# Kernel tuning notes

Measured on AMD Instinct MI355X. Metric: run time of the kernel, lower is better.

The kernel has to match this reference:

```python
import jax, jax.numpy as jnp
import numpy as np

LOCAL_HEADS = 8
GLOBAL_HEADS = 4
HEAD_DIM = 16  # dim // local_heads


def setup_inputs() -> dict:
    key = jax.random.key(0)
    ks = jax.random.split(key, 6)
    B, N, C = 8, 1024, 128
    gdim = HEAD_DIM * GLOBAL_HEADS  # 64
    return {
        "x": jax.random.normal(ks[0], (B, N, C), dtype=jnp.float32),
        "masks": jax.random.uniform(ks[1], (N, N, 3), dtype=jnp.float32),
        "Wq": jax.random.normal(ks[2], (gdim, C), dtype=jnp.float32) * 0.05,
        "Wk": jax.random.normal(ks[3], (gdim, C), dtype=jnp.float32) * 0.05,
        "Wv": jax.random.normal(ks[4], (C, C), dtype=jnp.float32) * 0.05,
        "mask_proj": jax.random.normal(ks[5], (3, GLOBAL_HEADS * LOCAL_HEADS), dtype=jnp.float32),
    }


def reference(x, masks, Wq, Wk, Wv, mask_proj):
    B, N, C = x.shape
    # projections (torch Linear: y = x @ W.T)
    q = (x @ Wq.T).reshape(B, N, GLOBAL_HEADS, HEAD_DIM)   # [B,N,G,hd]
    k = (x @ Wk.T).reshape(B, N, GLOBAL_HEADS, HEAD_DIM)
    v = (x @ Wv.T).reshape(B, N, LOCAL_HEADS, HEAD_DIM)    # [B,N,L,hd]
    # raw global-head scores: [B,G,N,N]  (no 1/sqrt(d) scaling in original)
    attn = jnp.einsum('bigd,bjgd->bgij', q, k)
    # learned mask mixing: masks [N,N,3] @ mask_proj [3, G*L] -> [N,N,G,L]
    mw = (masks @ mask_proj).reshape(N, N, GLOBAL_HEADS, LOCAL_HEADS)
    # mix global heads into local heads: [B,L,N,N]
    scores = jnp.einsum('bgij,ijgl->blij', attn, mw)
    probs = jax.nn.softmax(scores, axis=-1)               # over keys j
    out = jnp.einsum('blij,bjld->bild', probs, v)         # [B,N,L,hd]
    return out.reshape(B, N, C)
```

## Files before the change

kernel.cpp:

```cpp
#include <hip/hip_runtime.h>

#define BB 8
#define NN 1024
#define CC 128
#define GG 4
#define LL 8
#define GD 64

typedef __attribute__((ext_vector_type(8))) short short8;
typedef __attribute__((ext_vector_type(4))) short short4v;
typedef __attribute__((ext_vector_type(4))) float floatx4;

__device__ __forceinline__ short f2b(float f) {
  union { float f; unsigned u; } c; c.f = f;
  unsigned u = c.u;
  return (short)((u + 0x7FFFu + ((u >> 16) & 1u)) >> 16);
}
__device__ __forceinline__ float b2f(short s) {
  union { unsigned u; float f; } c; c.u = ((unsigned)(unsigned short)s) << 16;
  return c.f;
}
__device__ __forceinline__ void split2(float v, short& hi, short& lo) {
  short h = f2b(v);
  hi = h;
  lo = f2b(v - b2f(h));
}

#if __has_builtin(__builtin_amdgcn_cvt_pk_bf16_f32)
__device__ __forceinline__ unsigned pk2(float a, float b) {
  auto r = __builtin_amdgcn_cvt_pk_bf16_f32(a, b);
  unsigned u; __builtin_memcpy(&u, &r, 4); return u;
}
#else
__device__ __forceinline__ unsigned pk2(float a, float b) {
  return (unsigned)(unsigned short)f2b(a) | ((unsigned)(unsigned short)f2b(b) << 16);
}
#endif

#if __has_builtin(__builtin_amdgcn_exp2f)
#define EXP2(x) __builtin_amdgcn_exp2f(x)
#else
#define EXP2(x) exp2f(x)
#endif

#if __has_builtin(__builtin_amdgcn_global_load_lds)
__device__ __forceinline__ void gll16(const void* g, void* l, int lane) {
  (void)lane;
  __builtin_amdgcn_global_load_lds(
      (const __attribute__((address_space(1))) unsigned int*)g,
      (__attribute__((address_space(3))) unsigned int*)l, 16, 0, 0);
}
#else
__device__ __forceinline__ void gll16(const void* g, void* l, int lane) {
  uint4 t = *(const uint4*)g;
  *(uint4*)((char*)l + lane * 16) = t;
}
#endif

#define BHP 136

__global__ __launch_bounds__(256) void proj_kernel(
    const float* __restrict__ x, const float* __restrict__ Wq,
    const float* __restrict__ Wk, const float* __restrict__ Wv,
    short* __restrict__ qb, short* __restrict__ kb, short* __restrict__ vtb)
{
  __shared__ short bh[64 * BHP];
  __shared__ short bl[64 * BHP];
  const int t = threadIdx.x;
  const int nt = blockIdx.x & 3;
  const int mt = blockIdx.x >> 2;
  const int w = t >> 6;
  const int lane = t & 63;
  const int ln = lane & 15;
  const int hq = lane >> 4;
  const int arow = mt * 64 + w * 16 + ln;

  const float* wbase = (nt == 0) ? Wq : (nt == 1) ? Wk : (Wv + (nt - 2) * 64 * 128);

  {
    int r = t >> 2, c0 = (t & 3) * 32;
    const float* src = wbase + r * 128 + c0;
    #pragma unroll
    for (int z8 = 0; z8 < 4; ++z8) {
      float4 u0 = *(const float4*)(src + z8 * 8);
      float4 u1 = *(const float4*)(src + z8 * 8 + 4);
      float uv[8] = {u0.x,u0.y,u0.z,u0.w,u1.x,u1.y,u1.z,u1.w};
      union { short s[8]; short8 v; } H, L;
      #pragma unroll
      for (int z = 0; z < 8; ++z) split2(uv[z], H.s[z], L.s[z]);
      *(short8*)(bh + r * BHP + c0 + z8 * 8) = H.v;
      *(short8*)(bl + r * BHP + c0 + z8 * 8) = L.v;
    }
  }
  __syncthreads();

  const floatx4 zf = {0.f, 0.f, 0.f, 0.f};
  floatx4 acc[4] = {zf, zf, zf, zf};

  #pragma unroll
  for (int kc = 0; kc < 4; ++kc) {
    const float* xp = x + (long)arow * 128 + kc * 32 + hq * 8;
    float4 a0 = *(const float4*)xp;
    float4 a1 = *(const float4*)(xp + 4);
    union { short s[8]; short8 v; } Ah, Al;
    float av[8] = {a0.x,a0.y,a0.z,a0.w,a1.x,a1.y,a1.z,a1.w};
    #pragma unroll
    for (int z = 0; z < 8; ++z) split2(av[z], Ah.s[z], Al.s[z]);
    #pragma unroll
    for (int ns = 0; ns < 4; ++ns) {
      short8 Bh = *(const short8*)(bh + (ns * 16 + ln) * BHP + kc * 32 + hq * 8);
      short8 Bl = *(const short8*)(bl + (ns * 16 + ln) * BHP + kc * 32 + hq * 8);
      acc[ns] = __builtin_amdgcn_mfma_f32_16x16x32_bf16(Ah.v, Bh, acc[ns], 0,0,0);
      acc[ns] = __builtin_amdgcn_mfma_f32_16x16x32_bf16(Al.v, Bh, acc[ns], 0,0,0);
      acc[ns] = __builtin_amdgcn_mfma_f32_16x16x32_bf16(Ah.v, Bl, acc[ns], 0,0,0);
    }
  }

  if (nt < 2) {
    short* dst = (nt == 0) ? qb : kb;
    #pragma unroll
    for (int ns = 0; ns < 4; ++ns) {
      int col = ns * 16 + ln;
      #pragma unroll
      for (int reg = 0; reg < 4; ++reg) {
        int row = mt * 64 + w * 16 + hq * 4 + reg;
        dst[(long)row * 64 + col] = f2b(acc[ns][reg]);
      }
    }
  } else {
    int b = mt >> 4;
    int tok = (mt * 64 + w * 16 + hq * 4) & 1023;
    #pragma unroll
    for (int ns = 0; ns < 4; ++ns) {
      int cv = (nt - 2) * 64 + ns * 16 + ln;
      union { short s[4]; short4v v; } o;
      #pragma unroll
      for (int reg = 0; reg < 4; ++reg) o.s[reg] = f2b(acc[ns][reg]);
      *(short4v*)(vtb + ((long)b * CC + cv) * NN + tok) = o.v;
    }
  }
}

#define IT 16
#define JT 64
#define SPLIT 2
#define JSPAN 512
#define NTL 8
#define ARP 260
#define MRP 196

__global__ __launch_bounds__(256, 3) void attn_kernel(
    const short* __restrict__ qb, const short* __restrict__ kb,
    const short* __restrict__ vtb, const float* __restrict__ masks,
    const float* __restrict__ mask_proj,
    float* __restrict__ pnum, float* __restrict__ pden)
{
  __shared__ float arec[IT * ARP];
  __shared__ float mrec[IT * MRP];
  __shared__ short kbuf[64 * 64];

  const int t = threadIdx.x;
  const int sp = blockIdx.x & 1;
  const int itile = (blockIdx.x >> 1) & 63;
  const int b = blockIdx.x >> 7;
  const int i0 = itile * IT;

  const int w = t >> 6;
  const int lane = t & 63;
  const int ln = lane & 15;
  const int hq = lane >> 4;
  const int l0 = 2 * w, l1 = 2 * w + 1;

  short8 qf;
  {
    union { short s[8]; short8 v; } qq;
    #pragma unroll
    for (int z = 0; z < 8; ++z) qq.s[z] = 0;
    if (hq < 2)
      qq.v = *(const short8*)(qb + ((long)(b * NN + i0 + ln)) * GD + w * 16 + hq * 8);
    qf = qq.v;
  }
  const float LOG2E = 1.44269504088896340736f;
  float ycA[3][4], ycB[3][4];
  #pragma unroll
  for (int m = 0; m < 3; ++m)
    #pragma unroll
    for (int g = 0; g < 4; ++g) {
      ycA[m][g] = mask_proj[m * 32 + g * 8 + l0] * LOG2E;
      ycB[m][g] = mask_proj[m * 32 + g * 8 + l1] * LOG2E;
    }

  const floatx4 zf = {0.f, 0.f, 0.f, 0.f};
  floatx4 pv0 = zf, pv1 = zf;
  float den0 = 0.f, den1 = 0.f;

  const short* kbase = kb + (long)b * NN * GD;
  const short* v0base = vtb + ((long)b * CC + l0 * 16 + ln) * NN;
  const short* v1base = vtb + ((long)b * CC + l1 * 16 + ln) * NN;

  const int klj = lane >> 3;
  const int ke8 = (lane & 7) ^ klj;

  #pragma unroll
  for (int ii = 0; ii < 2; ++ii) {
    const int I = w * 2 + ii;
    gll16(kbase + (long)(sp * JSPAN + I * 8 + klj) * GD + ke8 * 8,
          kbuf + I * 512, lane);
  }

  for (int jt = 0; jt < NTL; ++jt) {
    const int j0 = sp * JSPAN + jt * JT;
    __syncthreads();

    #pragma unroll
    for (int it2 = 0; it2 < 3; ++it2) {
      int f = t + it2 * 256;
      int ii = f / 48;
      int rem = f - ii * 48;
      *(float4*)(mrec + ii * MRP + rem * 4) =
        *(const float4*)(masks + (long)(i0 + ii) * (NN * 3) + (long)j0 * 3 + rem * 4);
    }
    #pragma unroll
    for (int jsub = 0; jsub < 4; ++jsub) {
      union { short s[8]; short8 v; } kk;
      #pragma unroll
      for (int z = 0; z < 8; ++z) kk.s[z] = 0;
      if (hq < 2) {
        const int jloc = jsub * 16 + ln;
        kk.v = *(const short8*)(kbuf + jloc * 64 + (((w * 2 + hq) ^ (jloc & 7)) << 3));
      }
      floatx4 at = __builtin_amdgcn_mfma_f32_16x16x32_bf16(qf, kk.v, zf, 0, 0, 0);
      float* ab = arec + (jsub * 16 + ln) * 4 + w;
      #pragma unroll
      for (int reg = 0; reg < 4; ++reg)
        ab[(hq * 4 + reg) * ARP] = at[reg];
    }
    __syncthreads();

    {
      const int jn = sp * JSPAN + ((jt + 1) & (NTL - 1)) * JT;
      #pragma unroll
      for (int ii = 0; ii < 2; ++ii) {
        const int I = w * 2 + ii;
        gll16(kbase + (long)(jn + I * 8 + klj) * GD + ke8 * 8,
              kbuf + I * 512, lane);
      }
    }

    #pragma unroll
    for (int mf = 0; mf < 2; ++mf) {
      float mku[24];
      {
        const float* mb = mrec + ln * MRP + mf * 96 + hq * 24;
        #pragma unroll
        for (int q4 = 0; q4 < 6; ++q4)
          *(float4*)(mku + q4 * 4) = *(const float4*)(mb + q4 * 4);
      }
      short8 vf0 = *(const short8*)(v0base + j0 + mf * 32 + hq * 8);
      short8 vf1 = *(const short8*)(v1base + j0 + mf * 32 + hq * 8);
      const float* arA = arec + ln * ARP + (mf * 32 + hq * 8) * 4;
      union { unsigned u[4]; short8 v; } p0, p1;
      #pragma unroll
      for (int zp = 0; zp < 4; ++zp) {
        float eA[2], eB[2];
        #pragma unroll
        for (int zz = 0; zz < 2; ++zz) {
          int z = zp * 2 + zz;
          floatx4 a4 = *(const floatx4*)(arA + z * 4);
          float m0 = mku[z * 3], m1 = mku[z * 3 + 1], m2 = mku[z * 3 + 2];
          float wA0 = m0*ycA[0][0] + m1*ycA[1][0] + m2*ycA[2][0];
          float wA1 = m0*ycA[0][1] + m1*ycA[1][1] + m2*ycA[2][1];
          float wA2 = m0*ycA[0][2] + m1*ycA[1][2] + m2*ycA[2][2];
          float wA3 = m0*ycA[0][3] + m1*ycA[1][3] + m2*ycA[2][3];
          float wB0 = m0*ycB[0][0] + m1*ycB[1][0] + m2*ycB[2][0];
          float wB1 = m0*ycB[0][1] + m1*ycB[1][1] + m2*ycB[2][1];
          float wB2 = m0*ycB[0][2] + m1*ycB[1][2] + m2*ycB[2][2];
          float wB3 = m0*ycB[0][3] + m1*ycB[1][3] + m2*ycB[2][3];
          float sA = a4[0]*wA0 + a4[1]*wA1 + a4[2]*wA2 + a4[3]*wA3;
          float sB = a4[0]*wB0 + a4[1]*wB1 + a4[2]*wB2 + a4[3]*wB3;
          eA[zz] = EXP2(sA);
          eB[zz] = EXP2(sB);
        }
        den0 += eA[0] + eA[1];
        den1 += eB[0] + eB[1];
        p0.u[zp] = pk2(eA[0], eA[1]);
        p1.u[zp] = pk2(eB[0], eB[1]);
      }
      pv0 = __builtin_amdgcn_mfma_f32_16x16x32_bf16(p0.v, vf0, pv0, 0, 0, 0);
      pv1 = __builtin_amdgcn_mfma_f32_16x16x32_bf16(p1.v, vf1, pv1, 0, 0, 0);
    }
  }

  #pragma unroll
  for (int reg = 0; reg < 4; ++reg) {
    long row = ((long)(sp * BB + b)) * NN + i0 + hq * 4 + reg;
    pnum[row * CC + l0 * 16 + ln] = pv0[reg];
    pnum[row * CC + l1 * 16 + ln] = pv1[reg];
  }
  den0 += __shfl_xor(den0, 16, 64);
  den0 += __shfl_xor(den0, 32, 64);
  den1 += __shfl_xor(den1, 16, 64);
  den1 += __shfl_xor(den1, 32, 64);
  if (hq == 0) {
    long drow = ((long)(sp * BB + b)) * NN + i0 + ln;
    pden[drow * LL + l0] = den0;
    pden[drow * LL + l1] = den1;
  }
}

__global__ __launch_bounds__(256) void reduce_kernel(
    const float* __restrict__ pnum, const float* __restrict__ pden,
    float* __restrict__ out)
{
  int e4 = blockIdx.x * 256 + threadIdx.x;
  int bi = e4 >> 5;
  int l = (e4 & 31) >> 2;
  const float4* p4 = (const float4*)pnum;
  float4 n0 = p4[e4];
  float4 n1 = p4[e4 + (BB * NN * CC / 4)];
  float den = pden[(long)bi * LL + l] + pden[((long)BB * NN + bi) * LL + l];
  float inv = 1.0f / den;
  float4 o;
  o.x = (n0.x + n1.x) * inv;
  o.y = (n0.y + n1.y) * inv;
  o.z = (n0.z + n1.z) * inv;
  o.w = (n0.w + n1.w) * inv;
  ((float4*)out)[e4] = o;
}

extern "C" void kernel_launch(void* const* d_in, const int* in_sizes, int n_in,
                              void* d_out, int out_size, void* d_ws, size_t ws_size,
                              hipStream_t stream) {
  const float* x         = (const float*)d_in[0];
  const float* masks     = (const float*)d_in[1];
  const float* Wq        = (const float*)d_in[2];
  const float* Wk        = (const float*)d_in[3];
  const float* Wv        = (const float*)d_in[4];
  const float* mask_proj = (const float*)d_in[5];
  float* out = (float*)d_out;

  char* wsB = (char*)d_ws;
  short* qb   = (short*)(wsB);
  short* kb   = (short*)(wsB + (1l << 20));
  short* vtb  = (short*)(wsB + (2l << 20));
  float* pnum = (float*)(wsB + (4l << 20));
  float* pden = (float*)(wsB + (12l << 20));

  proj_kernel<<<512, 256, 0, stream>>>(x, Wq, Wk, Wv, qb, kb, vtb);
  attn_kernel<<<BB * (NN / IT) * SPLIT, 256, 0, stream>>>(qb, kb, vtb, masks,
                                                          mask_proj, pnum, pden);
  reduce_kernel<<<(BB * NN * CC / 4) / 256, 256, 0, stream>>>(pnum, pden, out);
}
```

Measured before the change: 127.4 us.

## Drop split-K over keys and reduce kernel; use 8 waves per block, one local head each

The attention kernel no longer splits the key range in two with partial numerators and denominators reduced by a separate kernel. Each block now has 512 threads covering the full key range, and each of the 8 waves handles one local head. Waves 4-7 load the mask tile while waves 0-3 compute the QK scores, and the kernel normalizes and writes the output directly. This removes the partial-sum writes, the reduce launch and its traffic, at the cost of half as many blocks and a longer serial loop per block.

```diff
diff --git a/kernel.cpp b/kernel.cpp
--- a/kernel.cpp
+++ b/kernel.cpp
@@ -143,108 +143,95 @@
 
 #define IT 16
 #define JT 64
-#define SPLIT 2
-#define JSPAN 512
-#define NTL 8
+#define NTL 16
 #define ARP 260
 #define MRP 196
 
-__global__ __launch_bounds__(256, 3) void attn_kernel(
+__global__ __launch_bounds__(512, 4) void attn_kernel(
     const short* __restrict__ qb, const short* __restrict__ kb,
     const short* __restrict__ vtb, const float* __restrict__ masks,
     const float* __restrict__ mask_proj,
-    float* __restrict__ pnum, float* __restrict__ pden)
+    float* __restrict__ out)
 {
   __shared__ float arec[IT * ARP];
   __shared__ float mrec[IT * MRP];
   __shared__ short kbuf[64 * 64];
 
   const int t = threadIdx.x;
-  const int sp = blockIdx.x & 1;
-  const int itile = (blockIdx.x >> 1) & 63;
-  const int b = blockIdx.x >> 7;
+  const int itile = blockIdx.x & 63;
+  const int b = blockIdx.x >> 6;
   const int i0 = itile * IT;
 
   const int w = t >> 6;
   const int lane = t & 63;
   const int ln = lane & 15;
   const int hq = lane >> 4;
-  const int l0 = 2 * w, l1 = 2 * w + 1;
+  const int t2 = t & 255;
 
   short8 qf;
   {
     union { short s[8]; short8 v; } qq;
     #pragma unroll
     for (int z = 0; z < 8; ++z) qq.s[z] = 0;
-    if (hq < 2)
+    if (w < 4 && hq < 2)
       qq.v = *(const short8*)(qb + ((long)(b * NN + i0 + ln)) * GD + w * 16 + hq * 8);
     qf = qq.v;
   }
   const float LOG2E = 1.44269504088896340736f;
-  float ycA[3][4], ycB[3][4];
+  float ycA[3][4];
   #pragma unroll
   for (int m = 0; m < 3; ++m)
     #pragma unroll
-    for (int g = 0; g < 4; ++g) {
-      ycA[m][g] = mask_proj[m * 32 + g * 8 + l0] * LOG2E;
-      ycB[m][g] = mask_proj[m * 32 + g * 8 + l1] * LOG2E;
-    }
+    for (int g = 0; g < 4; ++g)
+      ycA[m][g] = mask_proj[m * 32 + g * 8 + w] * LOG2E;
 
   const floatx4 zf = {0.f, 0.f, 0.f, 0.f};
-  floatx4 pv0 = zf, pv1 = zf;
-  float den0 = 0.f, den1 = 0.f;
+  floatx4 pv0 = zf;
+  float den0 = 0.f;
 
   const short* kbase = kb + (long)b * NN * GD;
-  const short* v0base = vtb + ((long)b * CC + l0 * 16 + ln) * NN;
-  const short* v1base = vtb + ((long)b * CC + l1 * 16 + ln) * NN;
+  const short* v0base = vtb + ((long)b * CC + w * 16 + ln) * NN;
 
   const int klj = lane >> 3;
   const int ke8 = (lane & 7) ^ klj;
 
-  #pragma unroll
-  for (int ii = 0; ii < 2; ++ii) {
-    const int I = w * 2 + ii;
-    gll16(kbase + (long)(sp * JSPAN + I * 8 + klj) * GD + ke8 * 8,
-          kbuf + I * 512, lane);
-  }
+  gll16(kbase + (long)(w * 8 + klj) * GD + ke8 * 8, kbuf + w * 512, lane);
 
   for (int jt = 0; jt < NTL; ++jt) {
-    const int j0 = sp * JSPAN + jt * JT;
+    const int j0 = jt * JT;
     __syncthreads();
 
-    #pragma unroll
-    for (int it2 = 0; it2 < 3; ++it2) {
-      int f = t + it2 * 256;
-      int ii = f / 48;
-      int rem = f - ii * 48;
-      *(float4*)(mrec + ii * MRP + rem * 4) =
-        *(const float4*)(masks + (long)(i0 + ii) * (NN * 3) + (long)j0 * 3 + rem * 4);
-    }
-    #pragma unroll
-    for (int jsub = 0; jsub < 4; ++jsub) {
-      union { short s[8]; short8 v; } kk;
-      #pragma unroll
-      for (int z = 0; z < 8; ++z) kk.s[z] = 0;
-      if (hq < 2) {
-        const int jloc = jsub * 16 + ln;
-        kk.v = *(const short8*)(kbuf + jloc * 64 + (((w * 2 + hq) ^ (jloc & 7)) << 3));
-      }
-      floatx4 at = __builtin_amdgcn_mfma_f32_16x16x32_bf16(qf, kk.v, zf, 0, 0, 0);
-      float* ab = arec + (jsub * 16 + ln) * 4 + w;
-      #pragma unroll
-      for (int reg = 0; reg < 4; ++reg)
-        ab[(hq * 4 + reg) * ARP] = at[reg];
+    if (w >= 4) {
+      #pragma unroll
+      for (int it2 = 0; it2 < 3; ++it2) {
+        int f = t2 + it2 * 256;
+        int ii = f / 48;
+        int rem = f - ii * 48;
+        *(float4*)(mrec + ii * MRP + rem * 4) =
+          *(const float4*)(masks + (long)(i0 + ii) * (NN * 3) + (long)j0 * 3 + rem * 4);
+      }
+    } else {
+      #pragma unroll
+      for (int jsub = 0; jsub < 4; ++jsub) {
+        union { short s[8]; short8 v; } kk;
+        #pragma unroll
+        for (int z = 0; z < 8; ++z) kk.s[z] = 0;
+        if (hq < 2) {
+          const int jloc = jsub * 16 + ln;
+          kk.v = *(const short8*)(kbuf + jloc * 64 + (((w * 2 + hq) ^ (jloc & 7)) << 3));
+        }
+        floatx4 at = __builtin_amdgcn_mfma_f32_16x16x32_bf16(qf, kk.v, zf, 0, 0, 0);
+        float* ab = arec + (jsub * 16 + ln) * 4 + w;
+        #pragma unroll
+        for (int reg = 0; reg < 4; ++reg)
+          ab[(hq * 4 + reg) * ARP] = at[reg];
+      }
     }
     __syncthreads();
 
     {
-      const int jn = sp * JSPAN + ((jt + 1) & (NTL - 1)) * JT;
-      #pragma unroll
-      for (int ii = 0; ii < 2; ++ii) {
-        const int I = w * 2 + ii;
-        gll16(kbase + (long)(jn + I * 8 + klj) * GD + ke8 * 8,
-              kbuf + I * 512, lane);
-      }
+      const int jn = ((jt + 1) & (NTL - 1)) * JT;
+      gll16(kbase + (long)(jn + w * 8 + klj) * GD + ke8 * 8, kbuf + w * 512, lane);
     }
 
     #pragma unroll
@@ -257,12 +244,11 @@
           *(float4*)(mku + q4 * 4) = *(const float4*)(mb + q4 * 4);
       }
       short8 vf0 = *(const short8*)(v0base + j0 + mf * 32 + hq * 8);
-      short8 vf1 = *(const short8*)(v1base + j0 + mf * 32 + hq * 8);
       const float* arA = arec + ln * ARP + (mf * 32 + hq * 8) * 4;
-      union { unsigned u[4]; short8 v; } p0, p1;
+      union { unsigned u[4]; short8 v; } p0;
       #pragma unroll
       for (int zp = 0; zp < 4; ++zp) {
-        float eA[2], eB[2];
+        float eA[2];
         #pragma unroll
         for (int zz = 0; zz < 2; ++zz) {
           int z = zp * 2 + zz;
@@ -272,60 +258,24 @@
           float wA1 = m0*ycA[0][1] + m1*ycA[1][1] + m2*ycA[2][1];
           float wA2 = m0*ycA[0][2] + m1*ycA[1][2] + m2*ycA[2][2];
           float wA3 = m0*ycA[0][3] + m1*ycA[1][3] + m2*ycA[2][3];
-          float wB0 = m0*ycB[0][0] + m1*ycB[1][0] + m2*ycB[2][0];
-          float wB1 = m0*ycB[0][1] + m1*ycB[1][1] + m2*ycB[2][1];
-          float wB2 = m0*ycB[0][2] + m1*ycB[1][2] + m2*ycB[2][2];
-          float wB3 = m0*ycB[0][3] + m1*ycB[1][3] + m2*ycB[2][3];
           float sA = a4[0]*wA0 + a4[1]*wA1 + a4[2]*wA2 + a4[3]*wA3;
-          float sB = a4[0]*wB0 + a4[1]*wB1 + a4[2]*wB2 + a4[3]*wB3;
           eA[zz] = EXP2(sA);
-          eB[zz] = EXP2(sB);
         }
         den0 += eA[0] + eA[1];
-        den1 += eB[0] + eB[1];
         p0.u[zp] = pk2(eA[0], eA[1]);
-        p1.u[zp] = pk2(eB[0], eB[1]);
       }
       pv0 = __builtin_amdgcn_mfma_f32_16x16x32_bf16(p0.v, vf0, pv0, 0, 0, 0);
-      pv1 = __builtin_amdgcn_mfma_f32_16x16x32_bf16(p1.v, vf1, pv1, 0, 0, 0);
-    }
-  }
-
+    }
+  }
+
+  den0 += __shfl_xor(den0, 16, 64);
+  den0 += __shfl_xor(den0, 32, 64);
   #pragma unroll
   for (int reg = 0; reg < 4; ++reg) {
-    long row = ((long)(sp * BB + b)) * NN + i0 + hq * 4 + reg;
-    pnum[row * CC + l0 * 16 + ln] = pv0[reg];
-    pnum[row * CC + l1 * 16 + ln] = pv1[reg];
-  }
-  den0 += __shfl_xor(den0, 16, 64);
-  den0 += __shfl_xor(den0, 32, 64);
-  den1 += __shfl_xor(den1, 16, 64);
-  den1 += __shfl_xor(den1, 32, 64);
-  if (hq == 0) {
-    long drow = ((long)(sp * BB + b)) * NN + i0 + ln;
-    pden[drow * LL + l0] = den0;
-    pden[drow * LL + l1] = den1;
-  }
-}
-
-__global__ __launch_bounds__(256) void reduce_kernel(
-    const float* __restrict__ pnum, const float* __restrict__ pden,
-    float* __restrict__ out)
-{
-  int e4 = blockIdx.x * 256 + threadIdx.x;
-  int bi = e4 >> 5;
-  int l = (e4 & 31) >> 2;
-  const float4* p4 = (const float4*)pnum;
-  float4 n0 = p4[e4];
-  float4 n1 = p4[e4 + (BB * NN * CC / 4)];
-  float den = pden[(long)bi * LL + l] + pden[((long)BB * NN + bi) * LL + l];
-  float inv = 1.0f / den;
-  float4 o;
-  o.x = (n0.x + n1.x) * inv;
-  o.y = (n0.y + n1.y) * inv;
-  o.z = (n0.z + n1.z) * inv;
-  o.w = (n0.w + n1.w) * inv;
-  ((float4*)out)[e4] = o;
+    float d = __shfl(den0, hq * 4 + reg, 64);
+    long row = (long)(b * NN + i0 + hq * 4 + reg);
+    out[row * CC + w * 16 + ln] = pv0[reg] / d;
+  }
 }
 
 extern "C" void kernel_launch(void* const* d_in, const int* in_sizes, int n_in,
@@ -343,11 +293,8 @@
   short* qb   = (short*)(wsB);
   short* kb   = (short*)(wsB + (1l << 20));
   short* vtb  = (short*)(wsB + (2l << 20));
-  float* pnum = (float*)(wsB + (4l << 20));
-  float* pden = (float*)(wsB + (12l << 20));
 
   proj_kernel<<<512, 256, 0, stream>>>(x, Wq, Wk, Wv, qb, kb, vtb);
-  attn_kernel<<<BB * (NN / IT) * SPLIT, 256, 0, stream>>>(qb, kb, vtb, masks,
-                                                          mask_proj, pnum, pden);
-  reduce_kernel<<<(BB * NN * CC / 4) / 256, 256, 0, stream>>>(pnum, pden, out);
-}
+  attn_kernel<<<BB * (NN / IT), 512, 0, stream>>>(qb, kb, vtb, masks,
+                                                  mask_proj, out);
+}
```

Result: slower. 137.8 us (+8.2%).
